# Performance work log

Measured on AMD Instinct MI355X. Metric: run time of the kernel, lower is better.

## Reference

```python
import jax, jax.numpy as jnp
import numpy as np

D = 256
H = 4
L = 6
N = 32768
NH = N // H  # 8192 per-head width
VOCAB = 256
B, T = 1, 1024
ROPE_BASE = 10000.0


def ln(x):
    # LayerNorm over last dim, no affine (elementwise_affine=False)
    m = jnp.mean(x, axis=-1, keepdims=True)
    v = jnp.var(x, axis=-1, keepdims=True)
    return (x - m) * jax.lax.rsqrt(v + 1e-5)


def rope(x):
    # standard rotary position embedding over the last dim (split-half convention)
    Dh = x.shape[-1]
    t = x.shape[-2]
    half = Dh // 2
    inv_freq = 1.0 / (ROPE_BASE ** (jnp.arange(half, dtype=jnp.float32) / half))
    ang = jnp.arange(t, dtype=jnp.float32)[:, None] * inv_freq[None, :]  # [T, half]
    cos, sin = jnp.cos(ang), jnp.sin(ang)
    x1, x2 = x[..., :half], x[..., half:]
    return jnp.concatenate([x1 * cos - x2 * sin, x2 * cos + x1 * sin], axis=-1)


def setup_inputs() -> dict:
    key = jax.random.key(0)
    ks = jax.random.split(key, 6)
    std = 0.02
    return {
        "idx": jax.random.randint(ks[0], (B, T), 0, VOCAB, dtype=jnp.int32),
        "wte": std * jax.random.normal(ks[1], (VOCAB, D), dtype=jnp.float32),
        "encoder": std * jax.random.normal(ks[2], (N, D), dtype=jnp.float32),
        "decoder_x": std * jax.random.normal(ks[3], (H, D, NH), dtype=jnp.float32),
        "decoder_y": std * jax.random.normal(ks[4], (H, D, NH), dtype=jnp.float32),
        "readout": std * jax.random.normal(ks[5], (D, VOCAB), dtype=jnp.float32),
    }


def reference(idx, wte, encoder, decoder_x, decoder_y, readout):
    b, t = idx.shape
    v = ln(wte[idx])  # [B, T, D]
    # strict causal mask (tril with diagonal=-1): position i attends to j < i
    mask = jnp.tril(jnp.ones((t, t), dtype=bool), k=-1)
    for _ in range(L):
        # x: relu(v @ decoder_x) -> [B, H, T, NH]
        x = jax.nn.relu(jnp.einsum('btd,hdn->bhtn', v, decoder_x))
        xr = rope(x)  # Q = K = x
        # unnormalized causal linear attention, strict lower triangular
        scores = jnp.einsum('bhtn,bhsn->bhts', xr, xr)
        scores = jnp.where(mask, scores, 0.0)
        a = jnp.einsum('bhts,bsd->bhtd', scores, v)  # V = v (broadcast over heads)
        # gated wide projection
        y = jax.nn.relu(jnp.einsum('bhtd,hdn->bhtn', ln(a), decoder_y)) * x
        # [B,H,T,NH] -> [B,T,H*NH] = [B,T,N]  (matches transpose(1,2).reshape)
        y = jnp.transpose(y, (0, 2, 1, 3)).reshape(b, t, N)
        v = ln(v + ln(y @ encoder))  # dropout is identity in eval
    return v @ readout  # [B, T, VOCAB]
```

## Files before the change

### kernel.cpp

```cpp
#include <hip/hip_runtime.h>
#include <hip/hip_bf16.h>
#include <stdint.h>

typedef unsigned short u16;
typedef unsigned int u32;
typedef __attribute__((ext_vector_type(8))) short i16x8;
typedef __attribute__((ext_vector_type(4))) float f32x4;

#define DEV __device__ __forceinline__

constexpr int T = 1024, D = 256, H = 4, NH = 8192, NF = 32768, HALF = 4096;

constexpr size_t OFF_DXT  = 0;
constexpr size_t OFF_DYT  = OFF_DXT  + (size_t)H*NH*D*2;
constexpr size_t OFF_ENCT = OFF_DYT  + (size_t)H*NH*D*2;
constexpr size_t OFF_ROT  = OFF_ENCT + (size_t)D*NF*2;
constexpr size_t OFF_COS  = OFF_ROT  + (size_t)D*D*2;
constexpr size_t OFF_SIN  = OFF_COS  + (size_t)T*HALF*4;
constexpr size_t OFF_V    = OFF_SIN  + (size_t)T*HALF*4;
constexpr size_t OFF_VBF  = OFF_V    + (size_t)T*D*4;
constexpr size_t OFF_VT   = OFF_VBF  + (size_t)T*D*2;
constexpr size_t OFF_X    = OFF_VT   + (size_t)T*D*2;
constexpr size_t OFF_XR   = OFF_X    + (size_t)T*NF*2;
constexpr size_t OFF_SC   = OFF_XR   + (size_t)T*NF*2;
constexpr size_t OFF_LA   = OFF_SC   + (size_t)H*T*T*2;
constexpr size_t OFF_PART = OFF_LA   + (size_t)H*T*D*2;
constexpr size_t WS_NEED  = OFF_PART + (size_t)8*T*T*4;

DEV u16 f2bf(float f) {
  u32 u = __float_as_uint(f);
  u += 0x7FFFu + ((u >> 16) & 1u);
  return (u16)(u >> 16);
}
DEV float bf2f(u16 u) { return __uint_as_float(((u32)u) << 16); }

DEV float2 block_sum2(float a, float b, float* sb) {
  #pragma unroll
  for (int o = 32; o > 0; o >>= 1) {
    a += __shfl_down(a, o, 64);
    b += __shfl_down(b, o, 64);
  }
  const int w = threadIdx.x >> 6;
  __syncthreads();
  if ((threadIdx.x & 63) == 0) { sb[w*2] = a; sb[w*2+1] = b; }
  __syncthreads();
  return make_float2(sb[0]+sb[2]+sb[4]+sb[6], sb[1]+sb[3]+sb[5]+sb[7]);
}

DEV void stage128(const u16* __restrict__ g, int ld, char* lds, int wave, int lane) {
  #pragma unroll
  for (int i = 0; i < 4; ++i) {
    const int f = (wave*4 + i)*64 + lane;
    const int row = f >> 3, seg = f & 7;
    const int segl = seg ^ (row & 7);
    const u16* src = g + (size_t)row*ld + segl*8;
    __builtin_amdgcn_global_load_lds(
        (const __attribute__((address_space(1))) void*)src,
        (__attribute__((address_space(3))) void*)(lds + ((wave*4 + i) << 10)),
        16, 0, 0);
  }
}

DEV void gemm_bt_core(const u16* __restrict__ Ab, int lda,
                      const u16* __restrict__ Bb, int ldb,
                      int nkt, char* smem, f32x4 acc[4][4]) {
  const int tid = threadIdx.x, lane = tid & 63, wave = tid >> 6;
  const int wm = wave >> 1, wn = wave & 1;
  const int lr = lane & 15, lk = lane >> 4;
  char* As = smem;
  char* Bs = smem + 32768;
  #pragma unroll
  for (int m = 0; m < 4; ++m)
    #pragma unroll
    for (int n = 0; n < 4; ++n) acc[m][n] = f32x4{0.f, 0.f, 0.f, 0.f};
  stage128(Ab, lda, As, wave, lane);
  stage128(Bb, ldb, Bs, wave, lane);
  __syncthreads();
  for (int kt = 0; kt < nkt; ++kt) {
    const int cur = kt & 1;
    if (kt + 1 < nkt) {
      stage128(Ab + (size_t)(kt+1)*64, lda, As + ((cur^1) << 14), wave, lane);
      stage128(Bb + (size_t)(kt+1)*64, ldb, Bs + ((cur^1) << 14), wave, lane);
    }
    const char* Ac = As + (cur << 14);
    const char* Bc = Bs + (cur << 14);
    #pragma unroll
    for (int kk = 0; kk < 2; ++kk) {
      const int lcol = kk*64 + lk*16;
      i16x8 af[4], bfv[4];
      #pragma unroll
      for (int m = 0; m < 4; ++m) {
        const int row = wm*64 + m*16 + lr;
        af[m] = *(const i16x8*)(Ac + row*128 + (lcol ^ ((row & 7) << 4)));
      }
      #pragma unroll
      for (int n = 0; n < 4; ++n) {
        const int row = wn*64 + n*16 + lr;
        bfv[n] = *(const i16x8*)(Bc + row*128 + (lcol ^ ((row & 7) << 4)));
      }
      #pragma unroll
      for (int m = 0; m < 4; ++m)
        #pragma unroll
        for (int n = 0; n < 4; ++n)
          acc[m][n] = __builtin_amdgcn_mfma_f32_16x16x32_bf16(af[m], bfv[n], acc[m][n], 0, 0, 0);
    }
    __syncthreads();
  }
}

#define EPILOG_IDX() \
  const int lane = threadIdx.x & 63, wave = threadIdx.x >> 6; \
  const int wm = wave >> 1, wn = wave & 1, lr = lane & 15, lk = lane >> 4; \
  const int r0 = wm*64 + lk*4; \
  const int c0 = wn*64 + lr;

constexpr int TS = 136;
template<int MODE>
DEV void store_tile(const f32x4 acc[4][4], u16* __restrict__ dst, int ld,
                    const u16* __restrict__ xg, char* smem) {
  u16* tb = (u16*)smem;
  EPILOG_IDX();
  #pragma unroll
  for (int m = 0; m < 4; ++m)
    #pragma unroll
    for (int n = 0; n < 4; ++n)
      #pragma unroll
      for (int r = 0; r < 4; ++r) {
        float v = acc[m][n][r];
        if (MODE >= 1) v = fmaxf(v, 0.f);
        tb[(size_t)(r0 + m*16 + r)*TS + c0 + n*16] = f2bf(v);
      }
  __syncthreads();
  const int rr = threadIdx.x >> 4;
  const int cc = (threadIdx.x & 15)*8;
  #pragma unroll
  for (int it = 0; it < 8; ++it) {
    const int row = it*16 + rr;
    i16x8 w = *(const i16x8*)(tb + (size_t)row*TS + cc);
    if (MODE == 2) {
      const i16x8 xv = *(const i16x8*)(xg + (size_t)row*ld + cc);
      #pragma unroll
      for (int j = 0; j < 8; ++j)
        w[j] = (short)f2bf(bf2f((u16)w[j]) * bf2f((u16)xv[j]));
    }
    *(i16x8*)(dst + (size_t)row*ld + cc) = w;
  }
}

__global__ __launch_bounds__(256) void k_transpose_cvt(const float* __restrict__ in,
                                                       u16* __restrict__ out, int R, int C) {
  __shared__ float tile[32][33];
  const size_t zoff = (size_t)blockIdx.z * R * C;
  const float* inz = in + zoff;
  u16* outz = out + zoff;
  const int c0 = blockIdx.x << 5, rr0 = blockIdx.y << 5;
  const int tx = threadIdx.x & 31, ty = threadIdx.x >> 5;
  #pragma unroll
  for (int i = 0; i < 4; ++i)
    tile[ty + i*8][tx] = inz[(size_t)(rr0 + ty + i*8)*C + c0 + tx];
  __syncthreads();
  #pragma unroll
  for (int i = 0; i < 4; ++i) {
    const int rr = ty + i*8;
    outz[(size_t)(c0 + rr)*R + rr0 + tx] = f2bf(tile[tx][rr]);
  }
}

__global__ __launch_bounds__(256) void k_rope_table(float* __restrict__ cosT,
                                                    float* __restrict__ sinT) {
  const int i = blockIdx.x*256 + threadIdx.x;
  const int t = blockIdx.y;
  const float p = (float)i * (1.f/4096.f);
  const float ang = (float)t * expf(-9.210340371976184f * p);
  cosT[(size_t)t*HALF + i] = cosf(ang);
  sinT[(size_t)t*HALF + i] = sinf(ang);
}

__global__ __launch_bounds__(256) void k_embed(const int* __restrict__ idx,
                                               const float* __restrict__ wte,
                                               float* __restrict__ v,
                                               u16* __restrict__ vbf, u16* __restrict__ vT) {
  __shared__ float sb[8];
  const int t = blockIdx.x, d = threadIdx.x;
  const float val = wte[(size_t)idx[t]*D + d];
  float2 ss = block_sum2(val, val*val, sb);
  const float m = ss.x*(1.f/256.f), var = ss.y*(1.f/256.f) - m*m;
  const float vn = (val - m) * rsqrtf(var + 1e-5f);
  v[(size_t)t*D + d] = vn;
  const u16 b = f2bf(vn);
  vbf[(size_t)t*D + d] = b;
  vT[(size_t)d*T + t] = b;
}

__global__ __launch_bounds__(256) void k_gemm_x_rope(const u16* __restrict__ vbf,
                                                     const u16* __restrict__ dxT,
                                                     u16* __restrict__ x,
                                                     u16* __restrict__ xr,
                                                     const float* __restrict__ cosT,
                                                     const float* __restrict__ sinT) {
  __shared__ char smem[65536];
  const int nt = blockIdx.x, mt = blockIdx.y, h = blockIdx.z;
  f32x4 acc1[4][4], acc2[4][4];
  gemm_bt_core(vbf + (size_t)mt*128*D, D,
               dxT + ((size_t)h*NH + (size_t)nt*128)*D, D, 4, smem, acc1);
  gemm_bt_core(vbf + (size_t)mt*128*D, D,
               dxT + ((size_t)h*NH + HALF + (size_t)nt*128)*D, D, 4, smem, acc2);
  u16* tb = (u16*)smem;
  const size_t obase = (size_t)mt*128*NF + (size_t)h*NH + (size_t)nt*128;
  {
    EPILOG_IDX();
    #pragma unroll
    for (int m = 0; m < 4; ++m)
      #pragma unroll
      for (int n = 0; n < 4; ++n)
        #pragma unroll
        for (int r = 0; r < 4; ++r)
          tb[(size_t)(r0 + m*16 + r)*TS + c0 + n*16] = f2bf(fmaxf(acc1[m][n][r], 0.f));
  }
  __syncthreads();
  const int rr = threadIdx.x >> 4;
  const int cc = (threadIdx.x & 15)*8;
  i16x8 w1[8];
  #pragma unroll
  for (int it = 0; it < 8; ++it) {
    const int row = it*16 + rr;
    w1[it] = *(const i16x8*)(tb + (size_t)row*TS + cc);
    *(i16x8*)(x + obase + (size_t)row*NF + cc) = w1[it];
  }
  __syncthreads();
  {
    EPILOG_IDX();
    #pragma unroll
    for (int m = 0; m < 4; ++m)
      #pragma unroll
      for (int n = 0; n < 4; ++n)
        #pragma unroll
        for (int r = 0; r < 4; ++r)
          tb[(size_t)(r0 + m*16 + r)*TS + c0 + n*16] = f2bf(fmaxf(acc2[m][n][r], 0.f));
  }
  __syncthreads();
  #pragma unroll
  for (int it = 0; it < 8; ++it) {
    const int row = it*16 + rr;
    const i16x8 w2 = *(const i16x8*)(tb + (size_t)row*TS + cc);
    *(i16x8*)(x + obase + (size_t)row*NF + HALF + cc) = w2;
    const int t = mt*128 + row;
    const int i = nt*128 + cc;
    float cb[8], sbv[8];
    *(float4*)cb       = *(const float4*)(cosT + (size_t)t*HALF + i);
    *(float4*)(cb+4)   = *(const float4*)(cosT + (size_t)t*HALF + i + 4);
    *(float4*)sbv      = *(const float4*)(sinT + (size_t)t*HALF + i);
    *(float4*)(sbv+4)  = *(const float4*)(sinT + (size_t)t*HALF + i + 4);
    i16x8 r1, r2;
    #pragma unroll
    for (int j = 0; j < 8; ++j) {
      const float x1 = bf2f((u16)w1[it][j]), x2 = bf2f((u16)w2[j]);
      r1[j] = (short)f2bf(x1*cb[j] - x2*sbv[j]);
      r2[j] = (short)f2bf(x2*cb[j] + x1*sbv[j]);
    }
    *(i16x8*)(xr + obase + (size_t)row*NF + cc) = r1;
    *(i16x8*)(xr + obase + (size_t)row*NF + HALF + cc) = r2;
  }
}

__global__ __launch_bounds__(256) void k_gemm_sc(const u16* __restrict__ xr,
                                                 u16* __restrict__ scb) {
  __shared__ char smem[65536];
  const int z = blockIdx.x & 15;
  const int i = blockIdx.x >> 4;
  int tt = 0;
  while ((tt + 1)*(tt + 2)/2 <= i) ++tt;
  const int st = i - tt*(tt + 1)/2;
  const int h = z >> 2, kc = z & 3;
  const u16* base = xr + (size_t)h*NH + (size_t)kc*2048;
  f32x4 acc[4][4];
  gemm_bt_core(base + (size_t)tt*128*NF, NF, base + (size_t)st*128*NF, NF, 32, smem, acc);
  store_tile<0>(acc, scb + (size_t)z*T*T + (size_t)tt*128*T + (size_t)st*128, T,
                nullptr, smem);
}

__global__ __launch_bounds__(256) void k_sc_combine(const u16* __restrict__ scb,
                                                    u16* __restrict__ sc) {
  const int row = blockIdx.x;
  const int h = row >> 10, t = row & 1023;
  const u16* p0 = scb + ((size_t)(h*4 + 0)*T + t)*T;
  u16* o = sc + (size_t)row*T;
  const int s0 = threadIdx.x*4;
  ushort4 r;
  if (s0 >= t) {
    r.x = 0; r.y = 0; r.z = 0; r.w = 0;
  } else {
    const ushort4 a0 = *(const ushort4*)(p0 + s0);
    const ushort4 a1 = *(const ushort4*)(p0 + T*T + s0);
    const ushort4 a2 = *(const ushort4*)(p0 + 2*(size_t)T*T + s0);
    const ushort4 a3 = *(const ushort4*)(p0 + 3*(size_t)T*T + s0);
    const float vx = bf2f(a0.x) + bf2f(a1.x) + bf2f(a2.x) + bf2f(a3.x);
    const float vy = bf2f(a0.y) + bf2f(a1.y) + bf2f(a2.y) + bf2f(a3.y);
    const float vz = bf2f(a0.z) + bf2f(a1.z) + bf2f(a2.z) + bf2f(a3.z);
    const float vw = bf2f(a0.w) + bf2f(a1.w) + bf2f(a2.w) + bf2f(a3.w);
    r.x = f2bf((s0 + 0 < t) ? vx : 0.f);
    r.y = f2bf((s0 + 1 < t) ? vy : 0.f);
    r.z = f2bf((s0 + 2 < t) ? vz : 0.f);
    r.w = f2bf((s0 + 3 < t) ? vw : 0.f);
  }
  *(ushort4*)(o + s0) = r;
}

__global__ __launch_bounds__(256) void k_gemm_av(const u16* __restrict__ sc,
                                                 const u16* __restrict__ vT,
                                                 float* __restrict__ part) {
  __shared__ char smem[65536];
  const int slot = blockIdx.x & 7;
  const int h = slot >> 1, nt = slot & 1;
  int mt = 0, kc = 0, rem = blockIdx.x >> 3;
  #pragma unroll
  for (int m = 0; m < 8; ++m) {
    const int c = (m >> 1) + 1;
    if (rem < c) { mt = m; kc = rem; break; }
    rem -= c;
  }
  f32x4 acc[4][4];
  gemm_bt_core(sc + ((size_t)h*T + (size_t)mt*128)*T + (size_t)kc*256, T,
               vT + (size_t)nt*128*T + (size_t)kc*256, T, 4, smem, acc);
  EPILOG_IDX();
  float* Cp = part + (size_t)(h*4 + kc) * T * D;
  const int tb = mt*128 + r0, cb = nt*128 + c0;
  #pragma unroll
  for (int m = 0; m < 4; ++m)
    #pragma unroll
    for (int n = 0; n < 4; ++n)
      #pragma unroll
      for (int r = 0; r < 4; ++r)
        Cp[(size_t)(tb + m*16 + r)*D + cb + n*16] = acc[m][n][r];
}

__global__ __launch_bounds__(256) void k_ln_a(const float* __restrict__ part,
                                              u16* __restrict__ la) {
  __shared__ float sb[8];
  const int row = blockIdx.x;
  const int h = row >> 10, t = row & 1023;
  const int d = threadIdx.x;
  const int nkc = ((t >> 7) >> 1) + 1;
  float s = 0.f;
  for (int kc = 0; kc < nkc; ++kc)
    s += part[((size_t)(h*4 + kc)*T + t)*D + d];
  float2 ss = block_sum2(s, s*s, sb);
  const float m = ss.x*(1.f/256.f), var = ss.y*(1.f/256.f) - m*m;
  la[(size_t)row*D + d] = f2bf((s - m) * rsqrtf(var + 1e-5f));
}

__global__ __launch_bounds__(256) void k_gemm_y(const u16* __restrict__ la,
                                                const u16* __restrict__ dyT,
                                                const u16* __restrict__ x,
                                                u16* __restrict__ y) {
  __shared__ char smem[65536];
  const int nt = blockIdx.x, mt = blockIdx.y, h = blockIdx.z;
  f32x4 acc[4][4];
  gemm_bt_core(la + ((size_t)h*T + (size_t)mt*128)*D, D,
               dyT + ((size_t)h*NH + (size_t)nt*128)*D, D, 4, smem, acc);
  const size_t off = (size_t)mt*128*NF + (size_t)h*NH + (size_t)nt*128;
  store_tile<2>(acc, y + off, NF, x + off, smem);
}

__global__ __launch_bounds__(256) void k_gemm_enc(const u16* __restrict__ y,
                                                  const u16* __restrict__ encT,
                                                  float* __restrict__ part) {
  __shared__ char smem[65536];
  const int slot = blockIdx.x & 7;
  const int seq  = blockIdx.x >> 3;
  const int kcc = slot*4 + (seq >> 4);
  const int nt = seq & 1;
  const int mt = (seq >> 1) & 7;
  f32x4 acc[4][4];
  gemm_bt_core(y + (size_t)mt*128*NF + (size_t)kcc*1024, NF,
               encT + (size_t)nt*128*NF + (size_t)kcc*1024, NF, 16, smem, acc);
  EPILOG_IDX();
  float* Cp = part + (size_t)kcc * T * D;
  const int tb = mt*128 + r0, cb = nt*128 + c0;
  #pragma unroll
  for (int m = 0; m < 4; ++m)
    #pragma unroll
    for (int n = 0; n < 4; ++n)
      #pragma unroll
      for (int r = 0; r < 4; ++r)
        Cp[(size_t)(tb + m*16 + r)*D + cb + n*16] = acc[m][n][r];
}

__global__ __launch_bounds__(256) void k_newv(const float* __restrict__ part,
                                              float* __restrict__ v,
                                              u16* __restrict__ vbf, u16* __restrict__ vT) {
  __shared__ float sb[8];
  const int t = blockIdx.x, d = threadIdx.x;
  float s = 0.f;
  #pragma unroll
  for (int kc = 0; kc < 32; ++kc)
    s += part[((size_t)kc*T + t)*D + d];
  float2 ss = block_sum2(s, s*s, sb);
  float m = ss.x*(1.f/256.f), var = ss.y*(1.f/256.f) - m*m;
  const float l1 = (s - m) * rsqrtf(var + 1e-5f);
  const float u = v[(size_t)t*D + d] + l1;
  float2 s2 = block_sum2(u, u*u, sb);
  m = s2.x*(1.f/256.f); var = s2.y*(1.f/256.f) - m*m;
  const float vn = (u - m) * rsqrtf(var + 1e-5f);
  v[(size_t)t*D + d] = vn;
  const u16 bb = f2bf(vn);
  vbf[(size_t)t*D + d] = bb;
  vT[(size_t)d*T + t] = bb;
}

__global__ __launch_bounds__(256) void k_gemm_out(const u16* __restrict__ vbf,
                                                  const u16* __restrict__ roT,
                                                  float* __restrict__ out) {
  __shared__ char smem[65536];
  const int nt = blockIdx.x, mt = blockIdx.y;
  f32x4 acc[4][4];
  gemm_bt_core(vbf + (size_t)mt*128*D, D, roT + (size_t)nt*128*D, D, 4, smem, acc);
  EPILOG_IDX();
  const int tb = mt*128 + r0, cb = nt*128 + c0;
  #pragma unroll
  for (int m = 0; m < 4; ++m)
    #pragma unroll
    for (int n = 0; n < 4; ++n)
      #pragma unroll
      for (int r = 0; r < 4; ++r)
        out[(size_t)(tb + m*16 + r)*D + cb + n*16] = acc[m][n][r];
}

extern "C" void kernel_launch(void* const* d_in, const int* in_sizes, int n_in,
                              void* d_out, int out_size, void* d_ws, size_t ws_size,
                              hipStream_t stream) {
  (void)in_sizes; (void)n_in; (void)out_size; (void)ws_size;
  const int*   idx = (const int*)d_in[0];
  const float* wte = (const float*)d_in[1];
  const float* enc = (const float*)d_in[2];
  const float* dx  = (const float*)d_in[3];
  const float* dy  = (const float*)d_in[4];
  const float* ro  = (const float*)d_in[5];
  float* out = (float*)d_out;
  char* ws = (char*)d_ws;

  u16* dxT  = (u16*)(ws + OFF_DXT);
  u16* dyT  = (u16*)(ws + OFF_DYT);
  u16* encT = (u16*)(ws + OFF_ENCT);
  u16* roT  = (u16*)(ws + OFF_ROT);
  float* cosT = (float*)(ws + OFF_COS);
  float* sinT = (float*)(ws + OFF_SIN);
  float* v    = (float*)(ws + OFF_V);
  u16* vbf  = (u16*)(ws + OFF_VBF);
  u16* vT   = (u16*)(ws + OFF_VT);
  u16* x    = (u16*)(ws + OFF_X);
  u16* xr   = (u16*)(ws + OFF_XR);
  u16* sc   = (u16*)(ws + OFF_SC);
  u16* la   = (u16*)(ws + OFF_LA);
  u16* scb  = (u16*)(ws + OFF_PART);
  float* part = (float*)(ws + OFF_PART);

  k_transpose_cvt<<<dim3(NH/32, D/32, H), 256, 0, stream>>>(dx, dxT, D, NH);
  k_transpose_cvt<<<dim3(NH/32, D/32, H), 256, 0, stream>>>(dy, dyT, D, NH);
  k_transpose_cvt<<<dim3(D/32, NF/32, 1), 256, 0, stream>>>(enc, encT, NF, D);
  k_transpose_cvt<<<dim3(D/32, D/32, 1), 256, 0, stream>>>(ro, roT, D, D);
  k_rope_table<<<dim3(HALF/256, T), 256, 0, stream>>>(cosT, sinT);
  k_embed<<<T, 256, 0, stream>>>(idx, wte, v, vbf, vT);

  for (int l = 0; l < 6; ++l) {
    k_gemm_x_rope<<<dim3(32, 8, H), 256, 0, stream>>>(vbf, dxT, x, xr, cosT, sinT);
    k_gemm_sc <<<576,              256, 0, stream>>>(xr, scb);
    k_sc_combine<<<H*T,            256, 0, stream>>>(scb, sc);
    k_gemm_av <<<160,              256, 0, stream>>>(sc, vT, part);
    k_ln_a    <<<H*T,              256, 0, stream>>>(part, la);
    k_gemm_y  <<<dim3(64, 8, H),   256, 0, stream>>>(la, dyT, x, xr );
    k_gemm_enc<<<512,              256, 0, stream>>>(xr , encT, part);
    k_newv    <<<T,                256, 0, stream>>>(part, v, vbf, vT);
  }
  k_gemm_out<<<dim3(2, 8), 256, 0, stream>>>(vbf, roT, out);
}
```

Measured before the change: 1.351 ms.

## Interleave RoPE half-pairs in feature layout to split x-GEMM into independent tiles

Permutes decoder_x and decoder_y columns so each rotary pair (i, i+4096) sits in adjacent columns, and permutes encoder rows to match. Each x-GEMM block then computes a single 128-wide tile and applies RoPE locally, instead of computing two tiles per block. The grid doubles, which should improve occupancy and parallelism and lower per-block register pressure. Downstream score, y and encoder contractions are unchanged because the same permutation is applied consistently, at the cost of more index math in the one-time weight transposes.

```diff
diff --git a/kernel.cpp b/kernel.cpp
--- a/kernel.cpp
+++ b/kernel.cpp
@@ -27,6 +27,7 @@
 constexpr size_t OFF_PART = OFF_LA   + (size_t)H*T*D*2;
 constexpr size_t WS_NEED  = OFF_PART + (size_t)8*T*T*4;
 
+
 DEV u16 f2bf(float f) {
   u32 u = __float_as_uint(f);
   u += 0x7FFFu + ((u >> 16) & 1u);
@@ -147,6 +148,7 @@
   }
 }
 
+template<int PERM>
 __global__ __launch_bounds__(256) void k_transpose_cvt(const float* __restrict__ in,
                                                        u16* __restrict__ out, int R, int C) {
   __shared__ float tile[32][33];
@@ -156,13 +158,24 @@
   const int c0 = blockIdx.x << 5, rr0 = blockIdx.y << 5;
   const int tx = threadIdx.x & 31, ty = threadIdx.x >> 5;
   #pragma unroll
-  for (int i = 0; i < 4; ++i)
-    tile[ty + i*8][tx] = inz[(size_t)(rr0 + ty + i*8)*C + c0 + tx];
+  for (int i = 0; i < 4; ++i) {
+    int irow = rr0 + ty + i*8;
+    if (PERM == 2) {
+      const int hh = irow >> 13, j = irow & 8191;
+      irow = hh*8192 + ((j & 1) ? (j >> 1) + 4096 : (j >> 1));
+    }
+    tile[ty + i*8][tx] = inz[(size_t)irow*C + c0 + tx];
+  }
   __syncthreads();
   #pragma unroll
   for (int i = 0; i < 4; ++i) {
     const int rr = ty + i*8;
-    outz[(size_t)(c0 + rr)*R + rr0 + tx] = f2bf(tile[tx][rr]);
+    int orow = c0 + rr;
+    if (PERM == 1) {
+      const int j = orow & 8191;
+      orow = (orow & ~8191) | ((j < 4096) ? 2*j : 2*(j - 4096) + 1);
+    }
+    outz[(size_t)orow*R + rr0 + tx] = f2bf(tile[tx][rr]);
   }
 }
 
@@ -200,13 +213,10 @@
                                                      const float* __restrict__ sinT) {
   __shared__ char smem[65536];
   const int nt = blockIdx.x, mt = blockIdx.y, h = blockIdx.z;
-  f32x4 acc1[4][4], acc2[4][4];
+  f32x4 acc[4][4];
   gemm_bt_core(vbf + (size_t)mt*128*D, D,
-               dxT + ((size_t)h*NH + (size_t)nt*128)*D, D, 4, smem, acc1);
-  gemm_bt_core(vbf + (size_t)mt*128*D, D,
-               dxT + ((size_t)h*NH + HALF + (size_t)nt*128)*D, D, 4, smem, acc2);
+               dxT + ((size_t)h*NH + (size_t)nt*128)*D, D, 4, smem, acc);
   u16* tb = (u16*)smem;
-  const size_t obase = (size_t)mt*128*NF + (size_t)h*NH + (size_t)nt*128;
   {
     EPILOG_IDX();
     #pragma unroll
@@ -215,51 +225,32 @@
       for (int n = 0; n < 4; ++n)
         #pragma unroll
         for (int r = 0; r < 4; ++r)
-          tb[(size_t)(r0 + m*16 + r)*TS + c0 + n*16] = f2bf(fmaxf(acc1[m][n][r], 0.f));
+          tb[(size_t)(r0 + m*16 + r)*TS + c0 + n*16] = f2bf(fmaxf(acc[m][n][r], 0.f));
   }
   __syncthreads();
   const int rr = threadIdx.x >> 4;
   const int cc = (threadIdx.x & 15)*8;
-  i16x8 w1[8];
+  const size_t obase = (size_t)mt*128*NF + (size_t)h*NH + (size_t)nt*128;
+  const int pbase = (nt*128 + cc) >> 1;
   #pragma unroll
   for (int it = 0; it < 8; ++it) {
     const int row = it*16 + rr;
-    w1[it] = *(const i16x8*)(tb + (size_t)row*TS + cc);
-    *(i16x8*)(x + obase + (size_t)row*NF + cc) = w1[it];
-  }
-  __syncthreads();
-  {
-    EPILOG_IDX();
-    #pragma unroll
-    for (int m = 0; m < 4; ++m)
-      #pragma unroll
-      for (int n = 0; n < 4; ++n)
-        #pragma unroll
-        for (int r = 0; r < 4; ++r)
-          tb[(size_t)(r0 + m*16 + r)*TS + c0 + n*16] = f2bf(fmaxf(acc2[m][n][r], 0.f));
-  }
-  __syncthreads();
-  #pragma unroll
-  for (int it = 0; it < 8; ++it) {
-    const int row = it*16 + rr;
-    const i16x8 w2 = *(const i16x8*)(tb + (size_t)row*TS + cc);
-    *(i16x8*)(x + obase + (size_t)row*NF + HALF + cc) = w2;
+    const i16x8 w = *(const i16x8*)(tb + (size_t)row*TS + cc);
+    *(i16x8*)(x + obase + (size_t)row*NF + cc) = w;
     const int t = mt*128 + row;
-    const int i = nt*128 + cc;
-    float cb[8], sbv[8];
-    *(float4*)cb       = *(const float4*)(cosT + (size_t)t*HALF + i);
-    *(float4*)(cb+4)   = *(const float4*)(cosT + (size_t)t*HALF + i + 4);
-    *(float4*)sbv      = *(const float4*)(sinT + (size_t)t*HALF + i);
-    *(float4*)(sbv+4)  = *(const float4*)(sinT + (size_t)t*HALF + i + 4);
-    i16x8 r1, r2;
-    #pragma unroll
-    for (int j = 0; j < 8; ++j) {
-      const float x1 = bf2f((u16)w1[it][j]), x2 = bf2f((u16)w2[j]);
-      r1[j] = (short)f2bf(x1*cb[j] - x2*sbv[j]);
-      r2[j] = (short)f2bf(x2*cb[j] + x1*sbv[j]);
-    }
-    *(i16x8*)(xr + obase + (size_t)row*NF + cc) = r1;
-    *(i16x8*)(xr + obase + (size_t)row*NF + HALF + cc) = r2;
+    const float4 cv = *(const float4*)(cosT + (size_t)t*HALF + pbase);
+    const float4 sv = *(const float4*)(sinT + (size_t)t*HALF + pbase);
+    i16x8 r;
+    float x1, x2;
+    x1 = bf2f((u16)w[0]); x2 = bf2f((u16)w[1]);
+    r[0] = (short)f2bf(x1*cv.x - x2*sv.x); r[1] = (short)f2bf(x2*cv.x + x1*sv.x);
+    x1 = bf2f((u16)w[2]); x2 = bf2f((u16)w[3]);
+    r[2] = (short)f2bf(x1*cv.y - x2*sv.y); r[3] = (short)f2bf(x2*cv.y + x1*sv.y);
+    x1 = bf2f((u16)w[4]); x2 = bf2f((u16)w[5]);
+    r[4] = (short)f2bf(x1*cv.z - x2*sv.z); r[5] = (short)f2bf(x2*cv.z + x1*sv.z);
+    x1 = bf2f((u16)w[6]); x2 = bf2f((u16)w[7]);
+    r[6] = (short)f2bf(x1*cv.w - x2*sv.w); r[7] = (short)f2bf(x2*cv.w + x1*sv.w);
+    *(i16x8*)(xr + obase + (size_t)row*NF + cc) = r;
   }
 }
 
@@ -455,15 +446,15 @@
   u16* scb  = (u16*)(ws + OFF_PART);
   float* part = (float*)(ws + OFF_PART);
 
-  k_transpose_cvt<<<dim3(NH/32, D/32, H), 256, 0, stream>>>(dx, dxT, D, NH);
-  k_transpose_cvt<<<dim3(NH/32, D/32, H), 256, 0, stream>>>(dy, dyT, D, NH);
-  k_transpose_cvt<<<dim3(D/32, NF/32, 1), 256, 0, stream>>>(enc, encT, NF, D);
-  k_transpose_cvt<<<dim3(D/32, D/32, 1), 256, 0, stream>>>(ro, roT, D, D);
+  k_transpose_cvt<1><<<dim3(NH/32, D/32, H), 256, 0, stream>>>(dx, dxT, D, NH);
+  k_transpose_cvt<1><<<dim3(NH/32, D/32, H), 256, 0, stream>>>(dy, dyT, D, NH);
+  k_transpose_cvt<2><<<dim3(D/32, NF/32, 1), 256, 0, stream>>>(enc, encT, NF, D);
+  k_transpose_cvt<0><<<dim3(D/32, D/32, 1), 256, 0, stream>>>(ro, roT, D, D);
   k_rope_table<<<dim3(HALF/256, T), 256, 0, stream>>>(cosT, sinT);
   k_embed<<<T, 256, 0, stream>>>(idx, wte, v, vbf, vT);
 
   for (int l = 0; l < 6; ++l) {
-    k_gemm_x_rope<<<dim3(32, 8, H), 256, 0, stream>>>(vbf, dxT, x, xr, cosT, sinT);
+    k_gemm_x_rope<<<dim3(64, 8, H), 256, 0, stream>>>(vbf, dxT, x, xr, cosT, sinT);
     k_gemm_sc <<<576,              256, 0, stream>>>(xr, scb);
     k_sc_combine<<<H*T,            256, 0, stream>>>(scb, sc);
     k_gemm_av <<<160,              256, 0, stream>>>(sc, vT, part);
```

Result: faster. 1.273 ms (-5.7%).
